# Performance work log

Hardware: AMD Instinct MI355X
Metric: run time of the kernel (lower is better)

Reference implementation:

```python
import jax, jax.numpy as jnp
import numpy as np

N_GAUSS = 1024
IMG_H = 128
IMG_W = 128
FOV_HALF = np.pi / 6.0  # 60 deg FOV
MIN_ALPHA = 1.0 / 255.0


def setup_inputs() -> dict:
    key = jax.random.key(0)
    k1, k2, k3, k4, k5 = jax.random.split(key, 5)
    # Gaussians placed in front of an identity camera looking down +z
    xy = jax.random.uniform(k1, (N_GAUSS, 2), minval=-3.0, maxval=3.0)
    z = jax.random.uniform(k2, (N_GAUSS, 1), minval=3.0, maxval=8.0)
    positions = jnp.concatenate([xy, z], axis=1).astype(jnp.float32)
    # PSD world-space covariances: A A^T + eps I
    A = jax.random.normal(k3, (N_GAUSS, 3, 3), dtype=jnp.float32) * 0.1
    covariances = jnp.einsum('nij,nkj->nik', A, A) + 0.01 * jnp.eye(3, dtype=jnp.float32)
    colors = jax.random.uniform(k4, (N_GAUSS, 3), dtype=jnp.float32)
    opacities = jax.random.uniform(k5, (N_GAUSS,), dtype=jnp.float32)
    camera_matrix = jnp.eye(4, dtype=jnp.float32)
    return {
        'positions': positions,
        'covariances': covariances,
        'colors': colors,
        'opacities': opacities,
        'camera_matrix': camera_matrix,
        'height': IMG_H,
        'width': IMG_W,
    }


def reference(positions, covariances, colors, opacities, camera_matrix, height, width):
    H, W = height, width
    focal = jnp.float32(0.5 * W / np.tan(FOV_HALF))
    # --- preprocess: project to camera space ---
    R = camera_matrix[:3, :3]
    t = camera_matrix[:3, 3]
    p_cam = positions @ R.T + t  # (N,3)
    x, y, z = p_cam[:, 0], p_cam[:, 1], p_cam[:, 2]
    zc = jnp.maximum(z, 1e-6)
    means_x = focal * x / zc + 0.5 * W
    means_y = focal * y / zc + 0.5 * H
    # perspective Jacobian (N,2,3) for EWA splatting
    zeros = jnp.zeros_like(zc)
    J = jnp.stack([
        jnp.stack([focal / zc, zeros, -focal * x / (zc * zc)], axis=-1),
        jnp.stack([zeros, focal / zc, -focal * y / (zc * zc)], axis=-1),
    ], axis=-2)
    covs = 0.5 * (covariances + jnp.swapaxes(covariances, -1, -2))
    cov_cam = jnp.einsum('ij,njk,lk->nil', R, covs, R)      # (N,3,3)
    cov2d = jnp.einsum('nij,njk,nlk->nil', J, cov_cam, J)   # (N,2,2)
    cov2d = cov2d + 0.3 * jnp.eye(2, dtype=cov2d.dtype)      # low-pass filter (3DGS)
    a = cov2d[:, 0, 0]; b = cov2d[:, 0, 1]; c = cov2d[:, 1, 1]
    det = a * c - b * b
    det_safe = jnp.where(det > 0, det, 1.0)
    conic_a = c / det_safe
    conic_b = -b / det_safe
    conic_c = a / det_safe
    valid = (z > 0.2) & (det > 0)
    # --- sort front-to-back by depth ---
    order = jnp.argsort(z)
    mx = means_x[order]; my = means_y[order]
    ca = conic_a[order]; cb = conic_b[order]; cc = conic_c[order]
    op = opacities[order]; col = colors[order]; vld = valid[order]
    # --- render: per-pixel alpha compositing (Algorithm 1) ---
    px = jnp.arange(W, dtype=jnp.float32) + 0.5
    py = jnp.arange(H, dtype=jnp.float32) + 0.5
    dx = px[None, None, :] - mx[:, None, None]  # (N,1,W)
    dy = py[None, :, None] - my[:, None, None]  # (N,H,1)
    power = -0.5 * (ca[:, None, None] * dx * dx + cc[:, None, None] * dy * dy) \
            - cb[:, None, None] * dx * dy        # (N,H,W)
    G = jnp.exp(jnp.minimum(power, 0.0))
    alpha = jnp.clip(op[:, None, None] * G, 0.0, 0.99)
    alpha = jnp.where(vld[:, None, None] & (alpha >= MIN_ALPHA), alpha, 0.0)
    # exclusive transmittance T_i = prod_{j<i} (1 - alpha_j)
    T = jnp.cumprod(1.0 - alpha, axis=0)
    T_excl = jnp.concatenate([jnp.ones((1, H, W), dtype=alpha.dtype), T[:-1]], axis=0)
    wgt = alpha * T_excl                          # (N,H,W)
    image = jnp.einsum('nhw,nc->hwc', wgt, col)   # (H,W,3)
    return image
```

## Files before the change

### kernel.cpp

```cpp
#include <hip/hip_runtime.h>
#include <math.h>

#define NG      1024
#define IMG_H   128
#define IMG_W   128
#define NPIX    (IMG_H * IMG_W)
#define MIN_A   (1.0f / 255.0f)
#define LOG2E   1.4426950408889634f


__global__ __launch_bounds__(1024) void gs_prep(
    const float* __restrict__ pos, const float* __restrict__ cov,
    const float* __restrict__ col, const float* __restrict__ opa,
    const float* __restrict__ cm,
    float4* __restrict__ g0, float4* __restrict__ g1, float* __restrict__ g2,
    float4* __restrict__ g3)
{
    __shared__ float zsh[NG];
    __shared__ int   prank[64][16];

    const int tid = threadIdx.x;
    const int b   = blockIdx.x;

    const float R20 = cm[8], R21 = cm[9], R22 = cm[10], T2 = cm[11];
    {
        const float p0 = pos[3*tid], p1 = pos[3*tid+1], p2 = pos[3*tid+2];
        zsh[tid] = fmaf(R20, p0, fmaf(R21, p1, fmaf(R22, p2, T2)));
    }
    __syncthreads();

    {
        const int g = tid & 15, q = tid >> 4;
        const int i = (b << 4) + g;
        const float zi = zsh[i];
        const float4* z4 = (const float4*)zsh;
        int r = 0;
        #pragma unroll
        for (int j4 = q * 4; j4 < q * 4 + 4; ++j4) {
            const float4 v = z4[j4];
            const int j = 4 * j4;
            r += (v.x < zi || (v.x == zi && j + 0 < i)) ? 1 : 0;
            r += (v.y < zi || (v.y == zi && j + 1 < i)) ? 1 : 0;
            r += (v.z < zi || (v.z == zi && j + 2 < i)) ? 1 : 0;
            r += (v.w < zi || (v.w == zi && j + 3 < i)) ? 1 : 0;
        }
        prank[q][g] = r;
    }
    __syncthreads();

    if (tid < 16) {
        const int g = tid;
        const int i = (b << 4) + g;

        int rank = 0;
        #pragma unroll
        for (int q = 0; q < 64; ++q) rank += prank[q][g];

        const float R00 = cm[0], R01 = cm[1], R02 = cm[2],  T0 = cm[3];
        const float R10 = cm[4], R11 = cm[5], R12 = cm[6],  T1 = cm[7];

        const float p0 = pos[3*i], p1 = pos[3*i+1], p2 = pos[3*i+2];
        const float x = R00*p0 + R01*p1 + R02*p2 + T0;
        const float y = R10*p0 + R11*p1 + R12*p2 + T1;
        const float z = zsh[i];

        const float focal = 110.85125168440814f;
        const float zc = fmaxf(z, 1e-6f);
        const float mx = focal * x / zc + 0.5f * IMG_W;
        const float my = focal * y / zc + 0.5f * IMG_H;

        const float c00 = cov[9*i+0], c01 = cov[9*i+1], c02 = cov[9*i+2];
        const float c10 = cov[9*i+3], c11 = cov[9*i+4], c12 = cov[9*i+5];
        const float c20 = cov[9*i+6], c21 = cov[9*i+7], c22 = cov[9*i+8];
        const float s00 = c00, s01 = 0.5f*(c01+c10), s02 = 0.5f*(c02+c20);
        const float s11 = c11, s12 = 0.5f*(c12+c21), s22 = c22;

        const float RS00 = R00*s00 + R01*s01 + R02*s02;
        const float RS01 = R00*s01 + R01*s11 + R02*s12;
        const float RS02 = R00*s02 + R01*s12 + R02*s22;
        const float RS10 = R10*s00 + R11*s01 + R12*s02;
        const float RS11 = R10*s01 + R11*s11 + R12*s12;
        const float RS12 = R10*s02 + R11*s12 + R12*s22;
        const float RS20 = R20*s00 + R21*s01 + R22*s02;
        const float RS21 = R20*s01 + R21*s11 + R22*s12;
        const float RS22 = R20*s02 + R21*s12 + R22*s22;
        const float CC00 = RS00*R00 + RS01*R01 + RS02*R02;
        const float CC01 = RS00*R10 + RS01*R11 + RS02*R12;
        const float CC02 = RS00*R20 + RS01*R21 + RS02*R22;
        const float CC11 = RS10*R10 + RS11*R11 + RS12*R12;
        const float CC12 = RS10*R20 + RS11*R21 + RS12*R22;
        const float CC20 = RS20*R00 + RS21*R01 + RS22*R02;
        const float CC21 = RS20*R10 + RS21*R11 + RS22*R12;
        const float CC22 = RS20*R20 + RS21*R21 + RS22*R22;

        const float j00 = focal / zc, j02 = -focal * x / (zc*zc);
        const float j11 = focal / zc, j12 = -focal * y / (zc*zc);

        const float v00 = CC00*j00 + CC02*j02;
        const float v02 = CC20*j00 + CC22*j02;
        const float v10 = CC01*j11 + CC02*j12;
        const float v11 = CC11*j11 + CC12*j12;
        const float v12 = CC21*j11 + CC22*j12;

        const float a  = j00*v00 + j02*v02 + 0.3f;
        const float bq = j00*v10 + j02*v12;
        const float cQ = j11*v11 + j12*v12 + 0.3f;

        const float det = a*cQ - bq*bq;
        const float det_safe = (det > 0.f) ? det : 1.f;
        const float conA =  cQ / det_safe;
        const float conB = -bq / det_safe;
        const float conC =  a  / det_safe;

        const bool  valid  = (z > 0.2f) && (det > 0.f);
        const float op_eff = valid ? opa[i] : 0.f;

        float dxm, dym;
        if (op_eff * 255.f > 1.f) {
            const float sN = logf(255.f * op_eff);
            dxm = sqrtf(2.f * sN * a)  * 1.001f + 0.06f;
            dym = sqrtf(2.f * sN * cQ) * 1.001f + 0.06f;
        } else {
            dxm = -1e30f; dym = -1e30f;
        }

        g0[rank] = make_float4(mx, my, -0.5f*conA*LOG2E, -conB*LOG2E);
        g1[rank] = make_float4(-0.5f*conC*LOG2E, op_eff, col[3*i], col[3*i+1]);
        g2[rank] = col[3*i+2];
        g3[rank] = make_float4(mx, my, dxm, dym);
    }
}

__global__ __launch_bounds__(1024) void gs_raster_tile(
    const float4* __restrict__ g0, const float4* __restrict__ g1,
    const float*  __restrict__ g2, const float4* __restrict__ g3,
    float* __restrict__ out)
{
    __shared__ float4 s0[NG];
    __shared__ float4 s1[NG];
    __shared__ float  s2[NG];
    __shared__ float4 part[16][64];

    const int tid = threadIdx.x;
    const float4 cl = g3[tid];
    s0[tid] = g0[tid];
    s1[tid] = g1[tid];
    s2[tid] = g2[tid];

    const int w    = tid >> 6;
    const int lane = tid & 63;
    const int tile = blockIdx.x;
    const float tx0 = (float)((tile & 15) << 3);
    const float ty0 = (float)((tile >> 4) << 3);

    const float pxf = tx0 + (float)(lane & 7) + 0.5f;
    const float pyf = ty0 + (float)(lane >> 3) + 0.5f;
    const float txl = tx0 + 0.5f, txh = tx0 + 7.5f;
    const float tyl = ty0 + 0.5f, tyh = ty0 + 7.5f;

    const bool hit = (cl.x - cl.z <= txh) && (cl.x + cl.z >= txl)
                  && (cl.y - cl.w <= tyh) && (cl.y + cl.w >= tyl);
    unsigned long long m = __ballot(hit);

    __syncthreads();

    const int base = w * 64;
    float T = 1.f, cr = 0.f, cg = 0.f, cb = 0.f;

    while (m) {
        const int i = __builtin_ctzll(m);
        m &= m - 1;
        const float4 A = s0[base + i];
        const float4 B = s1[base + i];
        const float  C = s2[base + i];
        const float dx = pxf - A.x;
        const float dy = pyf - A.y;
        const float pw = fminf(A.z*dx*dx + B.x*dy*dy + A.w*(dx*dy), 0.f);
        const float G = __builtin_amdgcn_exp2f(pw);
        float alpha = fminf(B.y * G, 0.99f);
        alpha = (alpha >= MIN_A) ? alpha : 0.f;
        const float wT = alpha * T;
        cr = fmaf(wT, B.z, cr);
        cg = fmaf(wT, B.w, cg);
        cb = fmaf(wT, C,   cb);
        T *= (1.f - alpha);
    }

    part[w][lane] = make_float4(cr, cg, cb, T);
    __syncthreads();

    if (tid < 64) {
        float Ts = 1.f, r = 0.f, g = 0.f, b = 0.f;
        #pragma unroll
        for (int k = 0; k < 16; ++k) {
            const float4 v = part[k][tid];
            r = fmaf(Ts, v.x, r);
            g = fmaf(Ts, v.y, g);
            b = fmaf(Ts, v.z, b);
            Ts *= v.w;
        }
        const int px = (int)tx0 + (tid & 7);
        const int py = (int)ty0 + (tid >> 3);
        float* o = out + 3 * (py * IMG_W + px);
        o[0] = r; o[1] = g; o[2] = b;
    }
}

extern "C" void kernel_launch(void* const* d_in, const int* in_sizes, int n_in,
                              void* d_out, int out_size, void* d_ws, size_t ws_size,
                              hipStream_t stream) {
    const float* pos = (const float*)d_in[0];
    const float* cov = (const float*)d_in[1];
    const float* col = (const float*)d_in[2];
    const float* opa = (const float*)d_in[3];
    const float* cm  = (const float*)d_in[4];

    char* ws = (char*)d_ws;
    float4* g0 = (float4*)(ws);
    float4* g1 = (float4*)(ws + 16384);
    float*  g2 = (float*) (ws + 32768);
    float4* g3 = (float4*)(ws + 36864);

    gs_prep<<<64, 1024, 0, stream>>>(pos, cov, col, opa, cm, g0, g1, g2, g3);
    gs_raster_tile<<<256, 1024, 0, stream>>>(g0, g1, g2, g3, (float*)d_out);
}
```

Measured before the change: 13.17 us.

## Fuse preprocessing and rasterization into one per-tile kernel with local hit sort

Merges the two kernels: every tile block recomputes the projection of all 1024 Gaussians into shared memory, builds a compacted list of the Gaussians hitting the tile with an atomic counter, and rank-sorts only that list by depth. The sorted hits are then split evenly across the 16 waves, where previously each wave scanned a fixed 64-Gaussian slice. This removes a kernel launch and the global-memory round trip, and balances per-wave work. In exchange every block repeats the preprocessing, runs an O(H^2) rank sort, and uses more shared memory, and the atomic-order hit list is only fixed up by the sort.

```diff
diff --git a/kernel.cpp b/kernel.cpp
--- a/kernel.cpp
+++ b/kernel.cpp
@@ -4,74 +4,52 @@
 #define NG      1024
 #define IMG_H   128
 #define IMG_W   128
-#define NPIX    (IMG_H * IMG_W)
 #define MIN_A   (1.0f / 255.0f)
 #define LOG2E   1.4426950408889634f
 
-
-__global__ __launch_bounds__(1024) void gs_prep(
+__global__ __launch_bounds__(1024) void gs_fused_tile(
     const float* __restrict__ pos, const float* __restrict__ cov,
     const float* __restrict__ col, const float* __restrict__ opa,
-    const float* __restrict__ cm,
-    float4* __restrict__ g0, float4* __restrict__ g1, float* __restrict__ g2,
-    float4* __restrict__ g3)
+    const float* __restrict__ cm, float* __restrict__ out)
 {
-    __shared__ float zsh[NG];
-    __shared__ int   prank[64][16];
+    __shared__ float  zsh[NG];
+    __shared__ float4 s0[NG];
+    __shared__ float4 s1[NG];
+    __shared__ float  s2[NG];
+    __shared__ int    hitlist[NG];
+    __shared__ float2 hzp[NG];
+    __shared__ int    order[NG];
+    __shared__ float4 part[16][64];
+    __shared__ int    hcnt;
 
-    const int tid = threadIdx.x;
-    const int b   = blockIdx.x;
+    const int tid  = threadIdx.x;
+    const int tile = blockIdx.x;
+    const float tx0 = (float)((tile & 15) << 3);
+    const float ty0 = (float)((tile >> 4) << 3);
+    const float txl = tx0 + 0.5f, txh = tx0 + 7.5f;
+    const float tyl = ty0 + 0.5f, tyh = ty0 + 7.5f;
 
-    const float R20 = cm[8], R21 = cm[9], R22 = cm[10], T2 = cm[11];
+    if (tid == 0) hcnt = 0;
+
+    bool hit;
     {
-        const float p0 = pos[3*tid], p1 = pos[3*tid+1], p2 = pos[3*tid+2];
-        zsh[tid] = fmaf(R20, p0, fmaf(R21, p1, fmaf(R22, p2, T2)));
-    }
-    __syncthreads();
-
-    {
-        const int g = tid & 15, q = tid >> 4;
-        const int i = (b << 4) + g;
-        const float zi = zsh[i];
-        const float4* z4 = (const float4*)zsh;
-        int r = 0;
-        #pragma unroll
-        for (int j4 = q * 4; j4 < q * 4 + 4; ++j4) {
-            const float4 v = z4[j4];
-            const int j = 4 * j4;
-            r += (v.x < zi || (v.x == zi && j + 0 < i)) ? 1 : 0;
-            r += (v.y < zi || (v.y == zi && j + 1 < i)) ? 1 : 0;
-            r += (v.z < zi || (v.z == zi && j + 2 < i)) ? 1 : 0;
-            r += (v.w < zi || (v.w == zi && j + 3 < i)) ? 1 : 0;
-        }
-        prank[q][g] = r;
-    }
-    __syncthreads();
-
-    if (tid < 16) {
-        const int g = tid;
-        const int i = (b << 4) + g;
-
-        int rank = 0;
-        #pragma unroll
-        for (int q = 0; q < 64; ++q) rank += prank[q][g];
-
         const float R00 = cm[0], R01 = cm[1], R02 = cm[2],  T0 = cm[3];
         const float R10 = cm[4], R11 = cm[5], R12 = cm[6],  T1 = cm[7];
+        const float R20 = cm[8], R21 = cm[9], R22 = cm[10], T2 = cm[11];
 
-        const float p0 = pos[3*i], p1 = pos[3*i+1], p2 = pos[3*i+2];
+        const float p0 = pos[3*tid], p1 = pos[3*tid+1], p2 = pos[3*tid+2];
         const float x = R00*p0 + R01*p1 + R02*p2 + T0;
         const float y = R10*p0 + R11*p1 + R12*p2 + T1;
-        const float z = zsh[i];
+        const float z = R20*p0 + R21*p1 + R22*p2 + T2;
 
         const float focal = 110.85125168440814f;
         const float zc = fmaxf(z, 1e-6f);
         const float mx = focal * x / zc + 0.5f * IMG_W;
         const float my = focal * y / zc + 0.5f * IMG_H;
 
-        const float c00 = cov[9*i+0], c01 = cov[9*i+1], c02 = cov[9*i+2];
-        const float c10 = cov[9*i+3], c11 = cov[9*i+4], c12 = cov[9*i+5];
-        const float c20 = cov[9*i+6], c21 = cov[9*i+7], c22 = cov[9*i+8];
+        const float c00 = cov[9*tid+0], c01 = cov[9*tid+1], c02 = cov[9*tid+2];
+        const float c10 = cov[9*tid+3], c11 = cov[9*tid+4], c12 = cov[9*tid+5];
+        const float c20 = cov[9*tid+6], c21 = cov[9*tid+7], c22 = cov[9*tid+8];
         const float s00 = c00, s01 = 0.5f*(c01+c10), s02 = 0.5f*(c02+c20);
         const float s11 = c11, s12 = 0.5f*(c12+c21), s22 = c22;
 
@@ -113,7 +91,7 @@
         const float conC =  a  / det_safe;
 
         const bool  valid  = (z > 0.2f) && (det > 0.f);
-        const float op_eff = valid ? opa[i] : 0.f;
+        const float op_eff = valid ? opa[tid] : 0.f;
 
         float dxm, dym;
         if (op_eff * 255.f > 1.f) {
@@ -124,55 +102,52 @@
             dxm = -1e30f; dym = -1e30f;
         }
 
-        g0[rank] = make_float4(mx, my, -0.5f*conA*LOG2E, -conB*LOG2E);
-        g1[rank] = make_float4(-0.5f*conC*LOG2E, op_eff, col[3*i], col[3*i+1]);
-        g2[rank] = col[3*i+2];
-        g3[rank] = make_float4(mx, my, dxm, dym);
+        zsh[tid] = z;
+        s0[tid] = make_float4(mx, my, -0.5f*conA*LOG2E, -conB*LOG2E);
+        s1[tid] = make_float4(-0.5f*conC*LOG2E, op_eff, col[3*tid], col[3*tid+1]);
+        s2[tid] = col[3*tid+2];
+
+        hit = (mx - dxm <= txh) && (mx + dxm >= txl)
+           && (my - dym <= tyh) && (my + dym >= tyl);
     }
-}
+    __syncthreads();
 
-__global__ __launch_bounds__(1024) void gs_raster_tile(
-    const float4* __restrict__ g0, const float4* __restrict__ g1,
-    const float*  __restrict__ g2, const float4* __restrict__ g3,
-    float* __restrict__ out)
-{
-    __shared__ float4 s0[NG];
-    __shared__ float4 s1[NG];
-    __shared__ float  s2[NG];
-    __shared__ float4 part[16][64];
+    if (hit) { const int p = atomicAdd(&hcnt, 1); hitlist[p] = tid; }
+    __syncthreads();
+    const int H = hcnt;
 
-    const int tid = threadIdx.x;
-    const float4 cl = g3[tid];
-    s0[tid] = g0[tid];
-    s1[tid] = g1[tid];
-    s2[tid] = g2[tid];
+    for (int k = tid; k < H; k += 1024) {
+        const int id = hitlist[k];
+        hzp[k] = make_float2(zsh[id], (float)id);
+    }
+    __syncthreads();
+
+    for (int k = tid; k < H; k += 1024) {
+        const float2 me = hzp[k];
+        int r = 0;
+        for (int j = 0; j < H; ++j) {
+            const float2 oz = hzp[j];
+            r += (oz.x < me.x || (oz.x == me.x && oz.y < me.y)) ? 1 : 0;
+        }
+        order[r] = (int)me.y;
+    }
+    __syncthreads();
 
     const int w    = tid >> 6;
     const int lane = tid & 63;
-    const int tile = blockIdx.x;
-    const float tx0 = (float)((tile & 15) << 3);
-    const float ty0 = (float)((tile >> 4) << 3);
-
     const float pxf = tx0 + (float)(lane & 7) + 0.5f;
     const float pyf = ty0 + (float)(lane >> 3) + 0.5f;
-    const float txl = tx0 + 0.5f, txh = tx0 + 7.5f;
-    const float tyl = ty0 + 0.5f, tyh = ty0 + 7.5f;
 
-    const bool hit = (cl.x - cl.z <= txh) && (cl.x + cl.z >= txl)
-                  && (cl.y - cl.w <= tyh) && (cl.y + cl.w >= tyl);
-    unsigned long long m = __ballot(hit);
+    const int C  = (H + 15) >> 4;
+    const int k0 = w * C;
+    const int k1 = (k0 + C < H) ? (k0 + C) : H;
 
-    __syncthreads();
-
-    const int base = w * 64;
     float T = 1.f, cr = 0.f, cg = 0.f, cb = 0.f;
-
-    while (m) {
-        const int i = __builtin_ctzll(m);
-        m &= m - 1;
-        const float4 A = s0[base + i];
-        const float4 B = s1[base + i];
-        const float  C = s2[base + i];
+    for (int k = k0; k < k1; ++k) {
+        const int id = order[k];
+        const float4 A  = s0[id];
+        const float4 B  = s1[id];
+        const float  Cc = s2[id];
         const float dx = pxf - A.x;
         const float dy = pyf - A.y;
         const float pw = fminf(A.z*dx*dx + B.x*dy*dy + A.w*(dx*dy), 0.f);
@@ -182,7 +157,7 @@
         const float wT = alpha * T;
         cr = fmaf(wT, B.z, cr);
         cg = fmaf(wT, B.w, cg);
-        cb = fmaf(wT, C,   cb);
+        cb = fmaf(wT, Cc,  cb);
         T *= (1.f - alpha);
     }
 
@@ -215,12 +190,6 @@
     const float* opa = (const float*)d_in[3];
     const float* cm  = (const float*)d_in[4];
 
-    char* ws = (char*)d_ws;
-    float4* g0 = (float4*)(ws);
-    float4* g1 = (float4*)(ws + 16384);
-    float*  g2 = (float*) (ws + 32768);
-    float4* g3 = (float4*)(ws + 36864);
-
-    gs_prep<<<64, 1024, 0, stream>>>(pos, cov, col, opa, cm, g0, g1, g2, g3);
-    gs_raster_tile<<<256, 1024, 0, stream>>>(g0, g1, g2, g3, (float*)d_out);
+    gs_fused_tile<<<256, 1024, 0, stream>>>(pos, cov, col, opa, cm,
+                                            (float*)d_out);
 }
```

Result: slower. 17.39 us (+32.1%).
